# Kernel tuning notes

Measured on AMD Instinct MI355X. Metric: run time of the kernel, lower is better.

Reference implementation:

```python
import jax, jax.numpy as jnp
import numpy as np

SCALES = (1, 3, 7, 15)
EPS_LN = 1e-5

def _layernorm(x, g, b):
    mu = jnp.mean(x, axis=-1, keepdims=True)
    var = jnp.mean(jnp.square(x - mu), axis=-1, keepdims=True)
    return (x - mu) / jnp.sqrt(var + EPS_LN) * g + b

def setup_inputs() -> dict:
    key = jax.random.key(0)
    ks = jax.random.split(key, 6)
    B, L, H, NL = 8, 4096, 1024, 4
    s = 0.02
    return {
        "sequence_features": jax.random.normal(ks[0], (B, L, H), jnp.float32),
        "hierarchy_masks": jax.random.uniform(ks[1], (B, L, NL), jnp.float32),
        "level_embeddings": jax.random.normal(ks[2], (NL, H), jnp.float32) * s,
        "lt_w": jax.random.normal(ks[3], (H, H), jnp.float32) * (1.0 / np.sqrt(H)),
        "lt_b": jnp.zeros((H,), jnp.float32),
        "ln1_g": jnp.ones((H,), jnp.float32),
        "ln1_b": jnp.zeros((H,), jnp.float32),
        "ft_w": jax.random.normal(ks[4], (H, H), jnp.float32) * (1.0 / np.sqrt(H)),
        "ft_b": jnp.zeros((H,), jnp.float32),
        "ln2_g": jnp.ones((H,), jnp.float32),
        "ln2_b": jnp.zeros((H,), jnp.float32),
    }

def _hierarchical_fusion(t, masks, level_emb, temperature=1.0):
    # t: [B,L,H], masks: [B,L,NL], level_emb: [NL,H]
    H = t.shape[-1]
    scores = jnp.einsum('blh,nh->bln', t, level_emb) / temperature      # [B,L,NL]
    keep = masks > 0.5
    w = jnp.where(keep, jnp.exp(scores), 0.0)                            # masked exp weights
    tot = jnp.sum(w, axis=-1, keepdims=True)                             # [B,L,1]
    fused = jnp.einsum('bln,nh->blh', w, level_emb)
    fused = jnp.where(tot > 1e-8, fused / jnp.where(tot > 1e-8, tot, 1.0), fused)
    gate = jax.nn.sigmoid(jnp.sum(fused * t, axis=-1, keepdims=True) / H)
    return gate * fused + (1.0 - gate) * t

def _multi_scale(x):
    # x: [B,L,H]; variable-window mean per scale via prefix sums
    B, L, H = x.shape
    csum = jnp.concatenate([jnp.zeros((B, 1, H), x.dtype), jnp.cumsum(x, axis=1)], axis=1)  # [B,L+1,H]
    pos = jnp.arange(L)
    agg = jnp.zeros_like(x)
    for scale in SCALES:
        start = jnp.clip(pos - scale // 2, 0, L)
        end = jnp.clip(pos + scale // 2 + 1, 0, L)
        wsum = jnp.take(csum, end, axis=1) - jnp.take(csum, start, axis=1)  # [B,L,H]
        cnt = (end - start).astype(x.dtype)[None, :, None]
        sw = 1.0 / (1.0 + np.log(float(scale)))
        agg = agg + sw * (wsum / cnt)
    return agg

def reference(sequence_features, hierarchy_masks, level_embeddings, lt_w, lt_b,
              ln1_g, ln1_b, ft_w, ft_b, ln2_g, ln2_b):
    t = _layernorm(sequence_features @ lt_w + lt_b, ln1_g, ln1_b)
    fused = _hierarchical_fusion(t, hierarchy_masks, level_embeddings)
    agg = _multi_scale(fused)
    out = _layernorm(agg @ ft_w + ft_b, ln2_g, ln2_b)
    return out + sequence_features
```

## Files before the change

kernel.cpp:

```cpp
#include <hip/hip_runtime.h>
#include <stdint.h>

typedef unsigned short u16;
typedef unsigned int u32;
typedef u16 u16x8 __attribute__((ext_vector_type(8)));
typedef u16 u16x4 __attribute__((ext_vector_type(4)));
typedef u16 u16x2 __attribute__((ext_vector_type(2)));
typedef __bf16 bf16x8 __attribute__((ext_vector_type(8)));
typedef float f32x4 __attribute__((ext_vector_type(4)));

__device__ __forceinline__ float bf2f(u16 u) {
    unsigned int x = ((unsigned int)u) << 16;
    float f; __builtin_memcpy(&f, &x, 4); return f;
}
__device__ __forceinline__ u16 f2bf(float f) {
    unsigned int x; __builtin_memcpy(&x, &f, 4);
    x += 0x7fffu + ((x >> 16) & 1u);
    return (u16)(x >> 16);
}
__device__ __forceinline__ float wsum(float v) {
#pragma unroll
    for (int o = 32; o > 0; o >>= 1) v += __shfl_xor(v, o, 64);
    return v;
}

__device__ __forceinline__ void gload16(const void* g, void* l) {
    const __attribute__((address_space(1))) u32* gp =
        reinterpret_cast<const __attribute__((address_space(1))) u32*>(
            reinterpret_cast<uintptr_t>(g));
    __attribute__((address_space(3))) u32* lp =
        reinterpret_cast<__attribute__((address_space(3))) u32*>(
            reinterpret_cast<uintptr_t>(l));
    __builtin_amdgcn_global_load_lds(gp, lp, 16, 0, 0);
}

template<int C_F32>
__global__ __launch_bounds__(256) void gemm_bt(
    const u16* __restrict__ A, const u16* __restrict__ Bt,
    void* __restrict__ Cp, int M, int N, int K)
{
    __shared__ __align__(16) u16 sA[128 * 32];
    __shared__ __align__(16) u16 sB[128 * 32];
    const int t = threadIdx.x;
    const int lane = t & 63, wave = t >> 6;
    const int quad = lane >> 4, lr = lane & 15;

    const int nwg = gridDim.x * gridDim.y;
    int id = blockIdx.y * gridDim.x + blockIdx.x;
    int swz = ((nwg & 7) == 0) ? ((id & 7) * (nwg >> 3) + (id >> 3)) : id;
    const int bx = swz % gridDim.x, by = swz / gridDim.x;
    const int m0 = by * 128, n0 = bx * 128;
    const int wm = (wave & 1) * 64, wn = (wave >> 1) * 64;

    const int r0 = t >> 2, kc = (t & 3) * 8;
    const u16* ga = A + (size_t)(m0 + r0) * K + kc;
    const u16* gb = Bt + (size_t)(n0 + r0) * K + kc;
    u16* la = sA + t * 8;
    u16* lb = sB + t * 8;
    const size_t rstride = (size_t)64 * K;

    f32x4 acc[4][4] = {};

    for (int kt = 0; kt < K; kt += 32) {
        __syncthreads();
        gload16(ga + kt, la);
        gload16(ga + kt + rstride, la + 2048);
        gload16(gb + kt, lb);
        gload16(gb + kt + rstride, lb + 2048);
        __syncthreads();

        bf16x8 af[4], bfr[4];
#pragma unroll
        for (int i = 0; i < 4; ++i)
            af[i] = *(const bf16x8*)(sA + (wm + i * 16 + lr) * 32 + quad * 8);
#pragma unroll
        for (int j = 0; j < 4; ++j)
            bfr[j] = *(const bf16x8*)(sB + (wn + j * 16 + lr) * 32 + quad * 8);
#pragma unroll
        for (int i = 0; i < 4; ++i)
#pragma unroll
            for (int j = 0; j < 4; ++j)
                acc[i][j] = __builtin_amdgcn_mfma_f32_16x16x32_bf16(af[i], bfr[j], acc[i][j], 0, 0, 0);
    }
#pragma unroll
    for (int i = 0; i < 4; ++i) {
        int mrow = m0 + wm + i * 16 + quad * 4;
#pragma unroll
        for (int j = 0; j < 4; ++j) {
            int ncol = n0 + wn + j * 16 + lr;
#pragma unroll
            for (int r = 0; r < 4; ++r) {
                if (C_F32) ((float*)Cp)[(size_t)(mrow + r) * N + ncol] = acc[i][j][r];
                else       ((u16*)Cp)[(size_t)(mrow + r) * N + ncol] = f2bf(acc[i][j][r]);
            }
        }
    }
}

__global__ __launch_bounds__(256) void f32_to_bf16(
    const float* __restrict__ in, u16* __restrict__ out, int n8)
{
    int i = blockIdx.x * 256 + threadIdx.x;
    const int stride = gridDim.x * 256;
    for (; i < n8; i += stride) {
        f32x4 a = *(const f32x4*)(in + (size_t)i * 8);
        f32x4 b = *(const f32x4*)(in + (size_t)i * 8 + 4);
        u16x8 o;
#pragma unroll
        for (int p = 0; p < 4; ++p) { o[p] = f2bf(a[p]); o[p + 4] = f2bf(b[p]); }
        *(u16x8*)(out + (size_t)i * 8) = o;
    }
}

__global__ __launch_bounds__(256) void w_transpose(
    const float* __restrict__ W, u16* __restrict__ Bt, int K, int N)
{
    __shared__ u16 tile[64][72];
    const int t = threadIdx.x;
    const int c4 = (t & 15) * 4;
    const int r0 = t >> 4;
    const int kb = blockIdx.y * 64, nb = blockIdx.x * 64;
#pragma unroll
    for (int p = 0; p < 4; ++p) {
        int k = p * 16 + r0;
        f32x4 v = *(const f32x4*)(W + (size_t)(kb + k) * N + nb + c4);
        u16x4 o;
#pragma unroll
        for (int j = 0; j < 4; ++j) o[j] = f2bf(v[j]);
        *(u16x4*)&tile[k][c4] = o;
    }
    __syncthreads();
#pragma unroll
    for (int p = 0; p < 4; ++p) {
        int n = p * 16 + r0;
        u16x4 o;
#pragma unroll
        for (int j = 0; j < 4; ++j) o[j] = tile[c4 + j][n];
        *(u16x4*)(Bt + (size_t)(nb + n) * K + kb + c4) = o;
    }
}

#define BM 128
#define BN 128
#define BKK 32
#define SBS (BN + 2)
template<int A_F32, int C_F32>
__global__ __launch_bounds__(256) void gemm_k(
    const void* __restrict__ Ap, const float* __restrict__ B,
    void* __restrict__ Cp, int M, int N, int K)
{
    __shared__ __align__(16) u16 sA[BM * BKK];
    __shared__ __align__(16) u16 sB[BKK * SBS];
    const int t = threadIdx.x;
    const int lane = t & 63, wave = t >> 6;
    const int m0 = blockIdx.y * BM, n0 = blockIdx.x * BN;
    const int wm = (wave & 1) * 64, wn = (wave >> 1) * 64;
    const int quad = lane >> 4, lr = lane & 15;

    f32x4 acc[4][4] = {};

    for (int kt = 0; kt < K; kt += BKK) {
        u16x8 va[2], vb[2];
#pragma unroll
        for (int r = 0; r < 2; ++r) {
            int c = t + r * 256;
            int arow = c >> 2, aks = (c & 3) * 8;
            if (A_F32) {
                const float* ga = (const float*)Ap + (size_t)(m0 + arow) * K + kt + aks;
                f32x4 f0 = *(const f32x4*)ga;
                f32x4 f1 = *(const f32x4*)(ga + 4);
#pragma unroll
                for (int p = 0; p < 4; ++p) { va[r][p] = f2bf(f0[p]); va[r][p + 4] = f2bf(f1[p]); }
            } else {
                va[r] = *(const u16x8*)((const u16*)Ap + (size_t)(m0 + arow) * K + kt + aks);
            }
            int bk = c >> 4, bn = (c & 15) * 8;
            const float* gb = B + (size_t)(kt + bk) * N + n0 + bn;
            f32x4 g0 = *(const f32x4*)gb;
            f32x4 g1 = *(const f32x4*)(gb + 4);
#pragma unroll
            for (int p = 0; p < 4; ++p) { vb[r][p] = f2bf(g0[p]); vb[r][p + 4] = f2bf(g1[p]); }
        }
        __syncthreads();
#pragma unroll
        for (int r = 0; r < 2; ++r) {
            int c = t + r * 256;
            *(u16x8*)((char*)sA + (size_t)c * 16) = va[r];
            int bk = c >> 4, bn = (c & 15) * 8;
            u16* dst = sB + bk * SBS + bn;
#pragma unroll
            for (int p = 0; p < 4; ++p) {
                u16x2 w; w[0] = vb[r][2 * p]; w[1] = vb[r][2 * p + 1];
                *(u16x2*)(dst + 2 * p) = w;
            }
        }
        __syncthreads();

        bf16x8 af[4], bfr[4];
#pragma unroll
        for (int i = 0; i < 4; ++i)
            af[i] = *(const bf16x8*)((const char*)sA + (wm + i * 16 + lr) * 64 + quad * 16);
#pragma unroll
        for (int i = 0; i < 4; ++i) {
            u16 tmp[8];
#pragma unroll
            for (int j = 0; j < 8; ++j)
                tmp[j] = sB[(quad * 8 + j) * SBS + (wn + i * 16 + lr)];
            __builtin_memcpy(&bfr[i], tmp, 16);
        }
#pragma unroll
        for (int i = 0; i < 4; ++i)
#pragma unroll
            for (int j = 0; j < 4; ++j)
                acc[i][j] = __builtin_amdgcn_mfma_f32_16x16x32_bf16(af[i], bfr[j], acc[i][j], 0, 0, 0);
    }
#pragma unroll
    for (int i = 0; i < 4; ++i) {
        int mrow = m0 + wm + i * 16 + quad * 4;
#pragma unroll
        for (int j = 0; j < 4; ++j) {
            int ncol = n0 + wn + j * 16 + lr;
#pragma unroll
            for (int r = 0; r < 4; ++r) {
                if (C_F32) ((float*)Cp)[(size_t)(mrow + r) * N + ncol] = acc[i][j][r];
                else       ((u16*)Cp)[(size_t)(mrow + r) * N + ncol] = f2bf(acc[i][j][r]);
            }
        }
    }
}

__global__ __launch_bounds__(256) void ln1_fusion(
    const u16* Y, const float* __restrict__ ltb,
    const float* __restrict__ g1, const float* __restrict__ b1,
    const float* __restrict__ masks, const float* __restrict__ emb,
    u16* fused, int ROWS)
{
    const int lane = threadIdx.x & 63;
    const int wid = blockIdx.x * (blockDim.x >> 6) + (threadIdx.x >> 6);
    const int nw = gridDim.x * (blockDim.x >> 6);
    const int h0 = lane * 16;

    float ltbv[16], gv[16], bv[16], ev[4][16];
#pragma unroll
    for (int i = 0; i < 16; ++i) {
        ltbv[i] = ltb[h0 + i];
        gv[i] = g1[h0 + i];
        bv[i] = b1[h0 + i];
    }
#pragma unroll
    for (int n = 0; n < 4; ++n)
#pragma unroll
        for (int i = 0; i < 16; ++i) ev[n][i] = emb[n * 1024 + h0 + i];

    for (int r = wid; r < ROWS; r += nw) {
        const u16* yrow = Y + (size_t)r * 1024 + h0;
        u16x8 v0 = *(const u16x8*)(yrow);
        u16x8 v1 = *(const u16x8*)(yrow + 8);
        float y[16], s = 0.f, sq = 0.f;
#pragma unroll
        for (int i = 0; i < 8; ++i) { y[i] = bf2f(v0[i]) + ltbv[i]; y[i + 8] = bf2f(v1[i]) + ltbv[i + 8]; }
#pragma unroll
        for (int i = 0; i < 16; ++i) { s += y[i]; sq += y[i] * y[i]; }
        s = wsum(s); sq = wsum(sq);
        float mu = s * (1.f / 1024.f);
        float var = fmaxf(sq * (1.f / 1024.f) - mu * mu, 0.f);
        float rinv = rsqrtf(var + 1e-5f);
        float tv[16];
#pragma unroll
        for (int i = 0; i < 16; ++i) tv[i] = (y[i] - mu) * rinv * gv[i] + bv[i];

        float p0 = 0.f, p1 = 0.f, p2 = 0.f, p3 = 0.f;
#pragma unroll
        for (int i = 0; i < 16; ++i) {
            p0 += tv[i] * ev[0][i]; p1 += tv[i] * ev[1][i];
            p2 += tv[i] * ev[2][i]; p3 += tv[i] * ev[3][i];
        }
        p0 = wsum(p0); p1 = wsum(p1); p2 = wsum(p2); p3 = wsum(p3);
        p0 = fminf(p0, 30.f); p1 = fminf(p1, 30.f); p2 = fminf(p2, 30.f); p3 = fminf(p3, 30.f);

        f32x4 mk = *(const f32x4*)(masks + (size_t)r * 4);
        float w0 = mk[0] > 0.5f ? expf(p0) : 0.f;
        float w1 = mk[1] > 0.5f ? expf(p1) : 0.f;
        float w2 = mk[2] > 0.5f ? expf(p2) : 0.f;
        float w3 = mk[3] > 0.5f ? expf(p3) : 0.f;
        float tot = w0 + w1 + w2 + w3;
        float inv = tot > 1e-8f ? 1.f / tot : 1.f;

        float fu[16], d = 0.f;
#pragma unroll
        for (int i = 0; i < 16; ++i) {
            fu[i] = (w0 * ev[0][i] + w1 * ev[1][i] + w2 * ev[2][i] + w3 * ev[3][i]) * inv;
            d += fu[i] * tv[i];
        }
        d = wsum(d);
        float gate = 1.f / (1.f + expf(fminf(-d * (1.f / 1024.f), 30.f)));

        u16x8 o0, o1;
#pragma unroll
        for (int i = 0; i < 8; ++i) {
            o0[i] = f2bf(gate * fu[i] + (1.f - gate) * tv[i]);
            o1[i] = f2bf(gate * fu[i + 8] + (1.f - gate) * tv[i + 8]);
        }
        u16* orow = fused + (size_t)r * 1024 + h0;
        *(u16x8*)(orow) = o0;
        *(u16x8*)(orow + 8) = o1;
    }
}

__global__ __launch_bounds__(256) void multiscale(
    const u16* __restrict__ fused, u16* __restrict__ agg, int L)
{
    const int bl = blockIdx.x;
    const int b = bl / L, l = bl - b * L;
    const int h0 = threadIdx.x * 4;

    const float sw[4] = { 1.f, 1.f / (1.f + logf(3.f)), 1.f / (1.f + logf(7.f)), 1.f / (1.f + logf(15.f)) };
    const int half[4] = { 0, 1, 3, 7 };
    float coef[4];
#pragma unroll
    for (int s = 0; s < 4; ++s) {
        int st = l - half[s]; if (st < 0) st = 0;
        int en = l + half[s] + 1; if (en > L) en = L;
        coef[s] = sw[s] / (float)(en - st);
    }
    float a0 = 0.f, a1 = 0.f, a2 = 0.f, a3 = 0.f;
#pragma unroll
    for (int d = -7; d <= 7; ++d) {
        int j = l + d;
        if ((unsigned)j >= (unsigned)L) continue;
        int ad = d < 0 ? -d : d;
        float c = coef[3];
        if (ad <= 3) c += coef[2];
        if (ad <= 1) c += coef[1];
        if (ad == 0) c += coef[0];
        u16x4 v = *(const u16x4*)(fused + ((size_t)(b * L + j)) * 1024 + h0);
        a0 += c * bf2f(v[0]); a1 += c * bf2f(v[1]);
        a2 += c * bf2f(v[2]); a3 += c * bf2f(v[3]);
    }
    u16x4 o; o[0] = f2bf(a0); o[1] = f2bf(a1); o[2] = f2bf(a2); o[3] = f2bf(a3);
    *(u16x4*)(agg + (size_t)bl * 1024 + h0) = o;
}

__global__ __launch_bounds__(256) void ln2_res(
    float* Y, const float* __restrict__ ftb,
    const float* __restrict__ g2, const float* __restrict__ b2,
    const float* __restrict__ x, int ROWS)
{
    const int lane = threadIdx.x & 63;
    const int wid = blockIdx.x * (blockDim.x >> 6) + (threadIdx.x >> 6);
    const int nw = gridDim.x * (blockDim.x >> 6);
    const int h0 = lane * 16;

    float ftbv[16], gv[16], bv[16];
#pragma unroll
    for (int i = 0; i < 16; ++i) {
        ftbv[i] = ftb[h0 + i];
        gv[i] = g2[h0 + i];
        bv[i] = b2[h0 + i];
    }
    for (int r = wid; r < ROWS; r += nw) {
        float* yrow = Y + (size_t)r * 1024 + h0;
        float y[16], s = 0.f, sq = 0.f;
#pragma unroll
        for (int q = 0; q < 4; ++q) {
            f32x4 v = *(const f32x4*)(yrow + 4 * q);
#pragma unroll
            for (int p = 0; p < 4; ++p) y[4 * q + p] = v[p] + ftbv[4 * q + p];
        }
#pragma unroll
        for (int i = 0; i < 16; ++i) { s += y[i]; sq += y[i] * y[i]; }
        s = wsum(s); sq = wsum(sq);
        float mu = s * (1.f / 1024.f);
        float var = fmaxf(sq * (1.f / 1024.f) - mu * mu, 0.f);
        float rinv = rsqrtf(var + 1e-5f);

        const float* xrow = x + (size_t)r * 1024 + h0;
#pragma unroll
        for (int q = 0; q < 4; ++q) {
            f32x4 xv = *(const f32x4*)(xrow + 4 * q);
            f32x4 o;
#pragma unroll
            for (int p = 0; p < 4; ++p)
                o[p] = (y[4 * q + p] - mu) * rinv * gv[4 * q + p] + bv[4 * q + p] + xv[p];
            *(f32x4*)(yrow + 4 * q) = o;
        }
    }
}

extern "C" void kernel_launch(void* const* d_in, const int* in_sizes, int n_in,
                              void* d_out, int out_size, void* d_ws, size_t ws_size,
                              hipStream_t stream) {
    const float* x     = (const float*)d_in[0];
    const float* masks = (const float*)d_in[1];
    const float* emb   = (const float*)d_in[2];
    const float* ltw   = (const float*)d_in[3];
    const float* ltb   = (const float*)d_in[4];
    const float* g1    = (const float*)d_in[5];
    const float* b1    = (const float*)d_in[6];
    const float* ftw   = (const float*)d_in[7];
    const float* ftb   = (const float*)d_in[8];
    const float* g2    = (const float*)d_in[9];
    const float* b2    = (const float*)d_in[10];
    float* out = (float*)d_out;

    const int H = 1024, L = 4096;
    const int M = in_sizes[0] / H;
    const size_t MB = 1024 * 1024;

    u16* plane0 = (u16*)d_out;
    u16* xbf    = (u16*)((char*)d_out + 64 * MB);
    u16* aggP   = (u16*)d_ws;
    const bool roomy = ws_size >= 68 * MB;
    u16* Bt1 = roomy ? (u16*)((char*)d_ws + 64 * MB) : (u16*)d_ws;
    u16* Bt2 = roomy ? (u16*)((char*)d_ws + 66 * MB) : nullptr;

    f32_to_bf16<<<2048, 256, 0, stream>>>(x, xbf, M * H / 8);
    w_transpose<<<dim3(16, 16), 256, 0, stream>>>(ltw, Bt1, H, H);
    if (roomy) w_transpose<<<dim3(16, 16), 256, 0, stream>>>(ftw, Bt2, H, H);

    gemm_bt<0><<<dim3(H / 128, M / 128), 256, 0, stream>>>(xbf, Bt1, plane0, M, H, H);
    ln1_fusion<<<1024, 256, 0, stream>>>(plane0, ltb, g1, b1, masks, emb, plane0, M);
    multiscale<<<M, 256, 0, stream>>>(plane0, aggP, L);
    if (roomy)
        gemm_bt<1><<<dim3(H / 128, M / 128), 256, 0, stream>>>(aggP, Bt2, out, M, H, H);
    else
        gemm_k<0, 1><<<dim3(H / BN, M / BM), 256, 0, stream>>>(aggP, ftw, out, M, H, H);
    ln2_res<<<1024, 256, 0, stream>>>(out, ftb, g2, b2, x, M);
}
```

Before: 672.8 us.

## Replace per-row multiscale kernel with LDS-staged sliding-window segment kernel

The multi-scale window-mean kernel now stages a 64-row segment plus a 14-row halo for half the hidden dimension into LDS. Each wave then computes 16 consecutive outputs with running sums for the 3-, 7- and 15-wide windows. Previously every output row re-read up to 15 neighbouring rows from global memory, so this cuts global traffic and arithmetic. The GEMM fallback template is specialised to bf16-in/f32-out and ln1_fusion is moved above it, neither of which changes behaviour.

```diff
diff --git a/kernel.cpp b/kernel.cpp
--- a/kernel.cpp
+++ b/kernel.cpp
@@ -140,14 +140,191 @@
     }
 }
 
+__global__ __launch_bounds__(256) void ln1_fusion(
+    const u16* Y, const float* __restrict__ ltb,
+    const float* __restrict__ g1, const float* __restrict__ b1,
+    const float* __restrict__ masks, const float* __restrict__ emb,
+    u16* fused, int ROWS)
+{
+    const int lane = threadIdx.x & 63;
+    const int wid = blockIdx.x * (blockDim.x >> 6) + (threadIdx.x >> 6);
+    const int nw = gridDim.x * (blockDim.x >> 6);
+    const int h0 = lane * 16;
+
+    float ltbv[16], gv[16], bv[16], ev[4][16];
+#pragma unroll
+    for (int i = 0; i < 16; ++i) {
+        ltbv[i] = ltb[h0 + i];
+        gv[i] = g1[h0 + i];
+        bv[i] = b1[h0 + i];
+    }
+#pragma unroll
+    for (int n = 0; n < 4; ++n)
+#pragma unroll
+        for (int i = 0; i < 16; ++i) ev[n][i] = emb[n * 1024 + h0 + i];
+
+    for (int r = wid; r < ROWS; r += nw) {
+        const u16* yrow = Y + (size_t)r * 1024 + h0;
+        u16x8 v0 = *(const u16x8*)(yrow);
+        u16x8 v1 = *(const u16x8*)(yrow + 8);
+        float y[16], s = 0.f, sq = 0.f;
+#pragma unroll
+        for (int i = 0; i < 8; ++i) { y[i] = bf2f(v0[i]) + ltbv[i]; y[i + 8] = bf2f(v1[i]) + ltbv[i + 8]; }
+#pragma unroll
+        for (int i = 0; i < 16; ++i) { s += y[i]; sq += y[i] * y[i]; }
+        s = wsum(s); sq = wsum(sq);
+        float mu = s * (1.f / 1024.f);
+        float var = fmaxf(sq * (1.f / 1024.f) - mu * mu, 0.f);
+        float rinv = rsqrtf(var + 1e-5f);
+        float tv[16];
+#pragma unroll
+        for (int i = 0; i < 16; ++i) tv[i] = (y[i] - mu) * rinv * gv[i] + bv[i];
+
+        float p0 = 0.f, p1 = 0.f, p2 = 0.f, p3 = 0.f;
+#pragma unroll
+        for (int i = 0; i < 16; ++i) {
+            p0 += tv[i] * ev[0][i]; p1 += tv[i] * ev[1][i];
+            p2 += tv[i] * ev[2][i]; p3 += tv[i] * ev[3][i];
+        }
+        p0 = wsum(p0); p1 = wsum(p1); p2 = wsum(p2); p3 = wsum(p3);
+        p0 = fminf(p0, 30.f); p1 = fminf(p1, 30.f); p2 = fminf(p2, 30.f); p3 = fminf(p3, 30.f);
+
+        f32x4 mk = *(const f32x4*)(masks + (size_t)r * 4);
+        float w0 = mk[0] > 0.5f ? expf(p0) : 0.f;
+        float w1 = mk[1] > 0.5f ? expf(p1) : 0.f;
+        float w2 = mk[2] > 0.5f ? expf(p2) : 0.f;
+        float w3 = mk[3] > 0.5f ? expf(p3) : 0.f;
+        float tot = w0 + w1 + w2 + w3;
+        float inv = tot > 1e-8f ? 1.f / tot : 1.f;
+
+        float fu[16], d = 0.f;
+#pragma unroll
+        for (int i = 0; i < 16; ++i) {
+            fu[i] = (w0 * ev[0][i] + w1 * ev[1][i] + w2 * ev[2][i] + w3 * ev[3][i]) * inv;
+            d += fu[i] * tv[i];
+        }
+        d = wsum(d);
+        float gate = 1.f / (1.f + expf(fminf(-d * (1.f / 1024.f), 30.f)));
+
+        u16x8 o0, o1;
+#pragma unroll
+        for (int i = 0; i < 8; ++i) {
+            o0[i] = f2bf(gate * fu[i] + (1.f - gate) * tv[i]);
+            o1[i] = f2bf(gate * fu[i + 8] + (1.f - gate) * tv[i + 8]);
+        }
+        u16* orow = fused + (size_t)r * 1024 + h0;
+        *(u16x8*)(orow) = o0;
+        *(u16x8*)(orow + 8) = o1;
+    }
+}
+
+#define MS_SEG 64
+#define MS_HH 512
+#define MS_ROWS (MS_SEG + 14)
+__global__ __launch_bounds__(256) void multiscale_slide(
+    const u16* __restrict__ fused, u16* __restrict__ agg, int L)
+{
+    __shared__ __align__(16) u16 sT[MS_ROWS * MS_HH];
+    const int t = threadIdx.x;
+    const int lane = t & 63, wave = t >> 6;
+    const int hhalf = blockIdx.x & 1;
+    const int bseg = blockIdx.x >> 1;
+    const int nseg = L / MS_SEG;
+    const int b = bseg / nseg, seg = bseg - b * nseg;
+    const int l0 = seg * MS_SEG;
+    const size_t base = (size_t)b * L * 1024 + (size_t)hhalf * MS_HH;
+
+    for (int r = wave; r < MS_ROWS; r += 4) {
+        int gl = l0 + r - 7;
+        u16x8 v = {};
+        if ((unsigned)gl < (unsigned)L)
+            v = *(const u16x8*)(fused + base + (size_t)gl * 1024 + lane * 8);
+        *(u16x8*)(sT + r * MS_HH + lane * 8) = v;
+    }
+    __syncthreads();
+
+    const int h0 = lane * 8;
+    const int lq = wave;
+    const u16* rowp = sT + (lq * 16) * MS_HH + h0;
+
+#define LOADR(dst, rr) { u16x8 _v = *(const u16x8*)(rowp + (rr) * MS_HH); \
+    _Pragma("unroll") for (int e = 0; e < 8; ++e) dst[e] = bf2f(_v[e]); }
+
+    float fc[8], a3[8], a7[8], a15[8];
+    {
+        float u[8], v[8];
+        LOADR(fc, 7);
+        LOADR(u, 6); LOADR(v, 8);
+#pragma unroll
+        for (int e = 0; e < 8; ++e) a3[e] = fc[e] + u[e] + v[e];
+        LOADR(u, 5); LOADR(v, 9);
+#pragma unroll
+        for (int e = 0; e < 8; ++e) a7[e] = a3[e] + u[e] + v[e];
+        LOADR(u, 4); LOADR(v, 10);
+#pragma unroll
+        for (int e = 0; e < 8; ++e) a7[e] += u[e] + v[e];
+        LOADR(u, 3); LOADR(v, 11);
+#pragma unroll
+        for (int e = 0; e < 8; ++e) a15[e] = a7[e] + u[e] + v[e];
+        LOADR(u, 2); LOADR(v, 12);
+#pragma unroll
+        for (int e = 0; e < 8; ++e) a15[e] += u[e] + v[e];
+        LOADR(u, 1); LOADR(v, 13);
+#pragma unroll
+        for (int e = 0; e < 8; ++e) a15[e] += u[e] + v[e];
+        LOADR(u, 0); LOADR(v, 14);
+#pragma unroll
+        for (int e = 0; e < 8; ++e) a15[e] += u[e] + v[e];
+    }
+
+    const float SW1 = 1.f / (1.f + logf(3.f));
+    const float SW2 = 1.f / (1.f + logf(7.f));
+    const float SW3 = 1.f / (1.f + logf(15.f));
+    const float C1 = SW1 / 3.f, C2 = SW2 / 7.f, C3 = SW3 / 15.f;
+
+    u16* outp = agg + base + (size_t)(l0 + lq * 16) * 1024 + h0;
+#pragma unroll
+    for (int i = 0; i < 16; ++i) {
+        const int l = l0 + lq * 16 + i;
+        float c1 = C1, c2 = C2, c3 = C3;
+        if (l < 7 || l + 7 >= L) {
+            int s1 = l - 1 < 0 ? 0 : l - 1, e1 = l + 2 > L ? L : l + 2;
+            int s2 = l - 3 < 0 ? 0 : l - 3, e2 = l + 4 > L ? L : l + 4;
+            int s3 = l - 7 < 0 ? 0 : l - 7, e3 = l + 8 > L ? L : l + 8;
+            c1 = SW1 / (float)(e1 - s1);
+            c2 = SW2 / (float)(e2 - s2);
+            c3 = SW3 / (float)(e3 - s3);
+        }
+        u16x8 o;
+#pragma unroll
+        for (int e = 0; e < 8; ++e)
+            o[e] = f2bf(fc[e] + c1 * a3[e] + c2 * a7[e] + c3 * a15[e]);
+        *(u16x8*)(outp + (size_t)i * 1024) = o;
+
+        if (i < 15) {
+            float p1[8], p2[8], m1[8], p4[8], m3[8], p8[8], m7[8];
+            LOADR(p1, 7 + i + 1); LOADR(p2, 7 + i + 2); LOADR(m1, 7 + i - 1);
+            LOADR(p4, 7 + i + 4); LOADR(m3, 7 + i - 3);
+            LOADR(p8, 7 + i + 8); LOADR(m7, 7 + i - 7);
+#pragma unroll
+            for (int e = 0; e < 8; ++e) {
+                a3[e]  += p2[e] - m1[e];
+                a7[e]  += p4[e] - m3[e];
+                a15[e] += p8[e] - m7[e];
+                fc[e]   = p1[e];
+            }
+        }
+    }
+#undef LOADR
+}
+
 #define BM 128
 #define BN 128
 #define BKK 32
 #define SBS (BN + 2)
-template<int A_F32, int C_F32>
-__global__ __launch_bounds__(256) void gemm_k(
-    const void* __restrict__ Ap, const float* __restrict__ B,
-    void* __restrict__ Cp, int M, int N, int K)
+__global__ __launch_bounds__(256) void gemm_k_bf_f32(
+    const u16* __restrict__ Ap, const float* __restrict__ B,
+    float* __restrict__ Cp, int M, int N, int K)
 {
     __shared__ __align__(16) u16 sA[BM * BKK];
     __shared__ __align__(16) u16 sB[BKK * SBS];
@@ -165,15 +342,7 @@
         for (int r = 0; r < 2; ++r) {
             int c = t + r * 256;
             int arow = c >> 2, aks = (c & 3) * 8;
-            if (A_F32) {
-                const float* ga = (const float*)Ap + (size_t)(m0 + arow) * K + kt + aks;
-                f32x4 f0 = *(const f32x4*)ga;
-                f32x4 f1 = *(const f32x4*)(ga + 4);
-#pragma unroll
-                for (int p = 0; p < 4; ++p) { va[r][p] = f2bf(f0[p]); va[r][p + 4] = f2bf(f1[p]); }
-            } else {
-                va[r] = *(const u16x8*)((const u16*)Ap + (size_t)(m0 + arow) * K + kt + aks);
-            }
+            va[r] = *(const u16x8*)(Ap + (size_t)(m0 + arow) * K + kt + aks);
             int bk = c >> 4, bn = (c & 15) * 8;
             const float* gb = B + (size_t)(kt + bk) * N + n0 + bn;
             f32x4 g0 = *(const f32x4*)gb;
@@ -221,124 +390,10 @@
         for (int j = 0; j < 4; ++j) {
             int ncol = n0 + wn + j * 16 + lr;
 #pragma unroll
-            for (int r = 0; r < 4; ++r) {
-                if (C_F32) ((float*)Cp)[(size_t)(mrow + r) * N + ncol] = acc[i][j][r];
-                else       ((u16*)Cp)[(size_t)(mrow + r) * N + ncol] = f2bf(acc[i][j][r]);
-            }
-        }
-    }
-}
-
-__global__ __launch_bounds__(256) void ln1_fusion(
-    const u16* Y, const float* __restrict__ ltb,
-    const float* __restrict__ g1, const float* __restrict__ b1,
-    const float* __restrict__ masks, const float* __restrict__ emb,
-    u16* fused, int ROWS)
-{
-    const int lane = threadIdx.x & 63;
-    const int wid = blockIdx.x * (blockDim.x >> 6) + (threadIdx.x >> 6);
-    const int nw = gridDim.x * (blockDim.x >> 6);
-    const int h0 = lane * 16;
-
-    float ltbv[16], gv[16], bv[16], ev[4][16];
-#pragma unroll
-    for (int i = 0; i < 16; ++i) {
-        ltbv[i] = ltb[h0 + i];
-        gv[i] = g1[h0 + i];
-        bv[i] = b1[h0 + i];
-    }
-#pragma unroll
-    for (int n = 0; n < 4; ++n)
-#pragma unroll
-        for (int i = 0; i < 16; ++i) ev[n][i] = emb[n * 1024 + h0 + i];
-
-    for (int r = wid; r < ROWS; r += nw) {
-        const u16* yrow = Y + (size_t)r * 1024 + h0;
-        u16x8 v0 = *(const u16x8*)(yrow);
-        u16x8 v1 = *(const u16x8*)(yrow + 8);
-        float y[16], s = 0.f, sq = 0.f;
-#pragma unroll
-        for (int i = 0; i < 8; ++i) { y[i] = bf2f(v0[i]) + ltbv[i]; y[i + 8] = bf2f(v1[i]) + ltbv[i + 8]; }
-#pragma unroll
-        for (int i = 0; i < 16; ++i) { s += y[i]; sq += y[i] * y[i]; }
-        s = wsum(s); sq = wsum(sq);
-        float mu = s * (1.f / 1024.f);
-        float var = fmaxf(sq * (1.f / 1024.f) - mu * mu, 0.f);
-        float rinv = rsqrtf(var + 1e-5f);
-        float tv[16];
-#pragma unroll
-        for (int i = 0; i < 16; ++i) tv[i] = (y[i] - mu) * rinv * gv[i] + bv[i];
-
-        float p0 = 0.f, p1 = 0.f, p2 = 0.f, p3 = 0.f;
-#pragma unroll
-        for (int i = 0; i < 16; ++i) {
-            p0 += tv[i] * ev[0][i]; p1 += tv[i] * ev[1][i];
-            p2 += tv[i] * ev[2][i]; p3 += tv[i] * ev[3][i];
-        }
-        p0 = wsum(p0); p1 = wsum(p1); p2 = wsum(p2); p3 = wsum(p3);
-        p0 = fminf(p0, 30.f); p1 = fminf(p1, 30.f); p2 = fminf(p2, 30.f); p3 = fminf(p3, 30.f);
-
-        f32x4 mk = *(const f32x4*)(masks + (size_t)r * 4);
-        float w0 = mk[0] > 0.5f ? expf(p0) : 0.f;
-        float w1 = mk[1] > 0.5f ? expf(p1) : 0.f;
-        float w2 = mk[2] > 0.5f ? expf(p2) : 0.f;
-        float w3 = mk[3] > 0.5f ? expf(p3) : 0.f;
-        float tot = w0 + w1 + w2 + w3;
-        float inv = tot > 1e-8f ? 1.f / tot : 1.f;
-
-        float fu[16], d = 0.f;
-#pragma unroll
-        for (int i = 0; i < 16; ++i) {
-            fu[i] = (w0 * ev[0][i] + w1 * ev[1][i] + w2 * ev[2][i] + w3 * ev[3][i]) * inv;
-            d += fu[i] * tv[i];
-        }
-        d = wsum(d);
-        float gate = 1.f / (1.f + expf(fminf(-d * (1.f / 1024.f), 30.f)));
-
-        u16x8 o0, o1;
-#pragma unroll
-        for (int i = 0; i < 8; ++i) {
-            o0[i] = f2bf(gate * fu[i] + (1.f - gate) * tv[i]);
-            o1[i] = f2bf(gate * fu[i + 8] + (1.f - gate) * tv[i + 8]);
-        }
-        u16* orow = fused + (size_t)r * 1024 + h0;
-        *(u16x8*)(orow) = o0;
-        *(u16x8*)(orow + 8) = o1;
-    }
-}
-
-__global__ __launch_bounds__(256) void multiscale(
-    const u16* __restrict__ fused, u16* __restrict__ agg, int L)
-{
-    const int bl = blockIdx.x;
-    const int b = bl / L, l = bl - b * L;
-    const int h0 = threadIdx.x * 4;
-
-    const float sw[4] = { 1.f, 1.f / (1.f + logf(3.f)), 1.f / (1.f + logf(7.f)), 1.f / (1.f + logf(15.f)) };
-    const int half[4] = { 0, 1, 3, 7 };
-    float coef[4];
-#pragma unroll
-    for (int s = 0; s < 4; ++s) {
-        int st = l - half[s]; if (st < 0) st = 0;
-        int en = l + half[s] + 1; if (en > L) en = L;
-        coef[s] = sw[s] / (float)(en - st);
-    }
-    float a0 = 0.f, a1 = 0.f, a2 = 0.f, a3 = 0.f;
-#pragma unroll
-    for (int d = -7; d <= 7; ++d) {
-        int j = l + d;
-        if ((unsigned)j >= (unsigned)L) continue;
-        int ad = d < 0 ? -d : d;
-        float c = coef[3];
-        if (ad <= 3) c += coef[2];
-        if (ad <= 1) c += coef[1];
-        if (ad == 0) c += coef[0];
-        u16x4 v = *(const u16x4*)(fused + ((size_t)(b * L + j)) * 1024 + h0);
-        a0 += c * bf2f(v[0]); a1 += c * bf2f(v[1]);
-        a2 += c * bf2f(v[2]); a3 += c * bf2f(v[3]);
-    }
-    u16x4 o; o[0] = f2bf(a0); o[1] = f2bf(a1); o[2] = f2bf(a2); o[3] = f2bf(a3);
-    *(u16x4*)(agg + (size_t)bl * 1024 + h0) = o;
+            for (int r = 0; r < 4; ++r)
+                Cp[(size_t)(mrow + r) * N + ncol] = acc[i][j][r];
+        }
+    }
 }
 
 __global__ __launch_bounds__(256) void ln2_res(
@@ -420,10 +475,10 @@
 
     gemm_bt<0><<<dim3(H / 128, M / 128), 256, 0, stream>>>(xbf, Bt1, plane0, M, H, H);
     ln1_fusion<<<1024, 256, 0, stream>>>(plane0, ltb, g1, b1, masks, emb, plane0, M);
-    multiscale<<<M, 256, 0, stream>>>(plane0, aggP, L);
+    multiscale_slide<<<(M / MS_SEG) * 2, 256, 0, stream>>>(plane0, aggP, L);
     if (roomy)
         gemm_bt<1><<<dim3(H / 128, M / 128), 256, 0, stream>>>(aggP, Bt2, out, M, H, H);
     else
-        gemm_k<0, 1><<<dim3(H / BN, M / BM), 256, 0, stream>>>(aggP, ftw, out, M, H, H);
+        gemm_k_bf_f32<<<dim3(H / BN, M / BM), 256, 0, stream>>>(aggP, ftw, out, M, H, H);
     ln2_res<<<1024, 256, 0, stream>>>(out, ftb, g2, b2, x, M);
 }
```

After: 586.3 us. 12.9% less time.
